# Performance work log

Measured on AMD Instinct MI355X. Metric: run time of the kernel, lower is better.

Reference implementation:

```python
import jax, jax.numpy as jnp
import numpy as np

B, E, S = 2, 1024, 2048
H = 16
D_QK = D_V = D_OUT = 1024
NEG = -1e4


def setup_inputs() -> dict:
    key = jax.random.key(0)
    ks = jax.random.split(key, 12)
    q = jax.random.normal(ks[0], (B, E, 1, S), jnp.float32)
    k = jax.random.normal(ks[1], (B, E, 1, S), jnp.float32)
    v = jax.random.normal(ks[2], (B, E, 1, S), jnp.float32)
    # causal qk_mask: (B, src, 1, tgt); src index > tgt index is masked
    causal = jnp.where(jnp.arange(S)[:, None] > jnp.arange(S)[None, :], NEG, 0.0).astype(jnp.float32)
    qk_mask = jnp.broadcast_to(causal[None, :, None, :], (B, S, 1, S))
    k_mask = jnp.zeros((B, S, 1, 1), jnp.float32)
    sc = 1.0 / np.sqrt(E)
    Wq = jax.random.normal(ks[3], (D_QK, E), jnp.float32) * sc
    Wk = jax.random.normal(ks[4], (D_QK, E), jnp.float32) * sc
    Wv = jax.random.normal(ks[5], (D_V, E), jnp.float32) * sc
    Wo = jax.random.normal(ks[6], (D_OUT, D_V), jnp.float32) * sc
    bq = jnp.zeros((D_QK,), jnp.float32)
    bk = jnp.zeros((D_QK,), jnp.float32)
    bv = jnp.zeros((D_V,), jnp.float32)
    bo = jnp.zeros((D_OUT,), jnp.float32)
    return {"q": q, "k": k, "v": v, "qk_mask": qk_mask, "k_mask": k_mask,
            "Wq": Wq, "bq": bq, "Wk": Wk, "bk": bk, "Wv": Wv, "bv": bv,
            "Wo": Wo, "bo": bo}


def reference(q, k, v, qk_mask, k_mask, Wq, bq, Wk, bk, Wv, bv, Wo, bo):
    b, _, _, tq = q.shape
    sk = k.shape[3]
    d_qk, d_v = Wq.shape[0], Wv.shape[0]
    dh, dvh = d_qk // H, d_v // H
    fact = float(dh) ** (-0.5)
    # 1x1 conv projections on (B, C, 1, S) == matmul over channels
    qp = jnp.einsum('oc,bcis->bois', Wq, q) + bq[None, :, None, None]
    kp = jnp.einsum('oc,bcis->bois', Wk, k) + bk[None, :, None, None]
    vp = jnp.einsum('oc,bcis->bois', Wv, v) + bv[None, :, None, None]
    # split heads: channel dim is head-major (contiguous chunks)
    qh = qp[:, :, 0, :].reshape(b, H, dh, tq)
    kh = kp[:, :, 0, :].reshape(b, H, dh, sk)
    vh = vp[:, :, 0, :].reshape(b, H, dvh, sk)
    # scores: (B, H, src, tgt); masks broadcast over heads
    scores = jnp.einsum('bhcq,bhck->bhkq', qh, kh) * fact
    scores = scores + qk_mask[:, None, :, 0, :] + k_mask[:, None, :, 0, 0][..., None]
    w = jax.nn.softmax(scores, axis=2)  # softmax over src (k) axis
    attn = jnp.einsum('bhkq,bhck->bhcq', w, vh).reshape(b, d_v, 1, tq)
    out = jnp.einsum('oc,bcis->bois', Wo, attn) + bo[None, :, None, None]
    return out
```

## Files before the change

### kernel.cpp

```cpp
#include <hip/hip_runtime.h>
#include <hip/hip_bf16.h>
#include <stdint.h>

typedef unsigned short u16;
typedef __attribute__((ext_vector_type(8))) short short8;
typedef __attribute__((ext_vector_type(4))) short short4v;
typedef __attribute__((ext_vector_type(4))) float f32x4;

#define MFMA16(a,b,c) __builtin_amdgcn_mfma_f32_16x16x32_bf16((a),(b),(c),0,0,0)
#define EXP2F(x) __builtin_amdgcn_exp2f(x)

typedef const __attribute__((address_space(1))) void glb_void;
typedef __attribute__((address_space(3))) void lds_void;

__device__ __forceinline__ u16 f2b(float f){
  unsigned u = __float_as_uint(f);
  u += 0x7fffu + ((u>>16)&1u);
  return (u16)(u>>16);
}
__device__ __forceinline__ unsigned pack_bf16(float a, float b){
  __hip_bfloat162 h = __float22bfloat162_rn(make_float2(a,b));
  unsigned u; __builtin_memcpy(&u, &h, 4); return u;
}
__device__ __forceinline__ void gld16(const void* g, void* l){
  __builtin_amdgcn_global_load_lds((glb_void*)g, (lds_void*)l, 16, 0, 0);
}

__device__ __forceinline__ void stage128x64_sw(const u16* g, u16* lds, int gstride, int w, int lane){
  const int sub = lane>>3, c16 = lane&7;
  const int gcol = (c16 ^ sub)<<3;
  #pragma unroll
  for (int i=0;i<4;++i){
    int r0 = (w*4+i)*8;
    gld16(g + (size_t)(r0 + sub)*gstride + gcol, lds + r0*64);
  }
}
__device__ __forceinline__ void stage64x64_sw(const u16* g, u16* lds, int gstride, int w, int lane){
  const int sub = lane>>3, c16 = lane&7;
  const int gcol = (c16 ^ sub)<<3;
  #pragma unroll
  for (int i=0;i<2;++i){
    int r0 = (w*2+i)*8;
    gld16(g + (size_t)(r0 + sub)*gstride + gcol, lds + r0*64);
  }
}
__device__ __forceinline__ const short8* frag64(const u16* lds, int row, int c16){
  return (const short8*)(lds + row*64 + ((c16 ^ (row&7))<<3));
}
__device__ __forceinline__ const short8* frag128(const u16* lds, int row, int c16){
  return (const short8*)(lds + row*128 + ((c16 ^ (row&15))<<3));
}

__global__ __launch_bounds__(256) void prep(
    const float* __restrict__ q, const float* __restrict__ k, const float* __restrict__ v,
    const float* __restrict__ qkm, const float* __restrict__ km,
    const float* __restrict__ Wq, const float* __restrict__ Wk,
    const float* __restrict__ Wv, const float* __restrict__ Wo,
    u16* __restrict__ W16, char* __restrict__ classes,
    u16* __restrict__ qT, u16* __restrict__ kT, u16* __restrict__ vT)
{
  __shared__ __align__(16) float t[64][72];
  const int bx = blockIdx.x, tid = threadIdx.x;
  const int S = 2048, E = 1024, nW = E*E;

  if (bx < 2048){
    const int sel = bx>>9, blk = bx&511;
    const float* src = sel==0?Wq : sel==1?Wk : sel==2?Wv : Wo;
    const float sc = (sel==0) ? 0.18033688f : 1.0f;
    u16* dst = W16 + (size_t)sel*nW;
    int i = (blk*256 + tid)*8;
    float4 a = *(const float4*)(src+i);
    float4 b = *(const float4*)(src+i+4);
    short8 o;
    o[0]=(short)f2b(a.x*sc); o[1]=(short)f2b(a.y*sc); o[2]=(short)f2b(a.z*sc); o[3]=(short)f2b(a.w*sc);
    o[4]=(short)f2b(b.x*sc); o[5]=(short)f2b(b.y*sc); o[6]=(short)f2b(b.z*sc); o[7]=(short)f2b(b.w*sc);
    *(short8*)(dst+i) = o;
  } else if (bx < 4096){
    const int tt = bx - 2048;
    const int b = tt>>10, qi = (tt>>5)&31, ki = tt&31;
    const int k0 = ki*64, q0 = qi*64;
    int az = 1, an = 1;
    #pragma unroll
    for (int p=0;p<4;++p){
      int e = tid + p*256;
      int row = e>>4, c4 = (e&15)*4;
      float kmv = km[(size_t)b*S + k0 + row];
      float4 mv = *(const float4*)&qkm[((size_t)b*S + k0 + row)*S + q0 + c4];
      mv.x += kmv; mv.y += kmv; mv.z += kmv; mv.w += kmv;
      az &= (mv.x==0.f) & (mv.y==0.f) & (mv.z==0.f) & (mv.w==0.f);
      an &= (mv.x<-1e3f) & (mv.y<-1e3f) & (mv.z<-1e3f) & (mv.w<-1e3f);
    }
    const int az_all = __syncthreads_and(az);
    const int an_all = __syncthreads_and(an);
    if (tid==0)
      classes[((size_t)b*32 + qi)*32 + ki] = an_all ? 2 : (az_all ? 0 : 1);
  } else {
    const int tt = bx - 4096;
    const int tensor = tt>>10, r = tt&1023;
    const int b = r>>9, rr = r&511;
    const int c0 = (rr>>5)*64, s0 = (rr&31)*64;
    const float* x = tensor==0 ? q : tensor==1 ? k : v;
    u16* xt = tensor==0 ? qT : tensor==1 ? kT : vT;
    #pragma unroll
    for (int p=0;p<4;++p){
      int e = tid + p*256;
      int row = e>>4, c4 = (e&15)*4;
      *(float4*)&t[row][c4] = *(const float4*)&x[((size_t)b*E + c0 + row)*S + s0 + c4];
    }
    __syncthreads();
    #pragma unroll
    for (int p=0;p<2;++p){
      int e = tid + p*256;
      int row = e>>3, col8 = (e&7)*8;
      short8 o;
      #pragma unroll
      for (int u=0;u<8;++u) o[u] = (short)f2b(t[col8+u][row]);
      *(short8*)&xt[((size_t)b*S + s0 + row)*E + c0 + col8] = o;
    }
  }
}

template<bool F32OUT>
__device__ __forceinline__ void gemm_core(
    const u16* __restrict__ A, const u16* __restrict__ Bt, const float* __restrict__ bias,
    float bscale, void* __restrict__ Cv, size_t cbase, int N, int K, int bias_on_m,
    int m0, int n0, u16* As, u16* Bs)
{
  const int tid = threadIdx.x, w = tid>>6, lane = tid&63;
  const int ln = lane&15, quad = lane>>4;
  const int m0w = (w>>1)*64, n0w = (w&1)*64;
  f32x4 acc[4][4];
  #pragma unroll
  for(int i=0;i<4;++i)
    #pragma unroll
    for(int j=0;j<4;++j) acc[i][j] = f32x4{0.f,0.f,0.f,0.f};

  for (int kc=0; kc<K; kc+=64){
    __syncthreads();
    stage128x64_sw(A  + (size_t)m0*K + kc, As, K, w, lane);
    stage128x64_sw(Bt + (size_t)n0*K + kc, Bs, K, w, lane);
    __syncthreads();
    #pragma unroll
    for (int kk=0; kk<64; kk+=32){
      const int c16 = (kk>>3) + quad;
      short8 af[4], bf[4];
      #pragma unroll
      for (int mt=0;mt<4;++mt) af[mt] = *frag64(As, m0w+mt*16+ln, c16);
      #pragma unroll
      for (int nt=0;nt<4;++nt) bf[nt] = *frag64(Bs, n0w+nt*16+ln, c16);
      #pragma unroll
      for (int mt=0;mt<4;++mt)
        #pragma unroll
        for (int nt=0;nt<4;++nt)
          acc[mt][nt] = MFMA16(af[mt], bf[nt], acc[mt][nt]);
    }
  }
  #pragma unroll
  for (int mt=0;mt<4;++mt){
    #pragma unroll
    for (int nt=0;nt<4;++nt){
      const int col = n0 + n0w + nt*16 + ln;
      const float bn = bias_on_m ? 0.f : bias[col]*bscale;
      #pragma unroll
      for (int r=0;r<4;++r){
        const int row = m0 + m0w + mt*16 + quad*4 + r;
        const float bb = bias_on_m ? bias[row]*bscale : bn;
        const float val = acc[mt][nt][r] + bb;
        const size_t idx = cbase + (size_t)row*N + col;
        if (F32OUT) ((float*)Cv)[idx] = val;
        else        ((u16*)Cv)[idx]   = f2b(val);
      }
    }
  }
}

__global__ __launch_bounds__(256,3) void proj(
    const u16* __restrict__ qT, const u16* __restrict__ kT, const u16* __restrict__ vT,
    const u16* __restrict__ W16,
    const float* __restrict__ bq, const float* __restrict__ bk, const float* __restrict__ bv,
    u16* __restrict__ Qb, u16* __restrict__ Kb, u16* __restrict__ Vb)
{
  __shared__ __align__(16) u16 As[128*64];
  __shared__ __align__(16) u16 Bs[128*64];
  const int bx = blockIdx.x;
  const int zone = bx>>7, r = bx&127;
  const size_t sSE = (size_t)2048*1024;
  const int nW = 1024*1024;
  if (zone < 4){
    const int sel = zone>>1, b = zone&1;
    const int m0 = (r>>3)*128, n0 = (r&7)*128;
    gemm_core<false>((sel? kT : qT) + b*sSE, W16 + (size_t)sel*nW, sel? bk : bq,
                     sel? 1.0f : 0.18033688f, sel? Kb : Qb, b*sSE,
                     1024, 1024, 0, m0, n0, As, Bs);
  } else {
    const int b = zone&1;
    const int m0 = (r>>4)*128, n0 = (r&15)*128;
    gemm_core<false>(W16 + (size_t)2*nW, vT + b*sSE, bv,
                     1.0f, Vb, b*sSE,
                     2048, 1024, 1, m0, n0, As, Bs);
  }
}

__global__ __launch_bounds__(256,4) void gemm_out64(
    const u16* __restrict__ Wo16, const u16* __restrict__ At, const float* __restrict__ bo,
    float* __restrict__ out)
{
  __shared__ __align__(16) u16 As[64*64];
  __shared__ __align__(16) u16 Bs[128*64];
  const int b = blockIdx.z;
  const int m0 = blockIdx.y*64, n0 = blockIdx.x*128;
  const size_t sSE = (size_t)2048*1024;
  const int K = 1024, N = 2048;
  const u16* Bt = At + b*sSE;
  const int tid = threadIdx.x, w = tid>>6, lane = tid&63;
  const int ln = lane&15, quad = lane>>4;
  const int m0w = (w>>1)*32, n0w = (w&1)*64;
  f32x4 acc[2][4];
  #pragma unroll
  for(int i=0;i<2;++i)
    #pragma unroll
    for(int j=0;j<4;++j) acc[i][j] = f32x4{0.f,0.f,0.f,0.f};

  for (int kc=0; kc<K; kc+=64){
    __syncthreads();
    stage64x64_sw (Wo16 + (size_t)m0*K + kc, As, K, w, lane);
    stage128x64_sw(Bt   + (size_t)n0*K + kc, Bs, K, w, lane);
    __syncthreads();
    #pragma unroll
    for (int kk=0; kk<64; kk+=32){
      const int c16 = (kk>>3) + quad;
      short8 af[2], bf[4];
      #pragma unroll
      for (int mt=0;mt<2;++mt) af[mt] = *frag64(As, m0w+mt*16+ln, c16);
      #pragma unroll
      for (int nt=0;nt<4;++nt) bf[nt] = *frag64(Bs, n0w+nt*16+ln, c16);
      #pragma unroll
      for (int mt=0;mt<2;++mt)
        #pragma unroll
        for (int nt=0;nt<4;++nt)
          acc[mt][nt] = MFMA16(af[mt], bf[nt], acc[mt][nt]);
    }
  }
  #pragma unroll
  for (int mt=0;mt<2;++mt){
    #pragma unroll
    for (int nt=0;nt<4;++nt){
      const int col = n0 + n0w + nt*16 + ln;
      #pragma unroll
      for (int r=0;r<4;++r){
        const int row = m0 + m0w + mt*16 + quad*4 + r;
        out[b*sSE + (size_t)row*N + col] = acc[mt][nt][r] + bo[row];
      }
    }
  }
}

__global__ __launch_bounds__(256,2) void attn(
    const u16* __restrict__ Qb, const u16* __restrict__ Kb, const u16* __restrict__ Vb,
    const float* __restrict__ qk_mask, const float* __restrict__ k_mask,
    const char* __restrict__ classes, u16* __restrict__ Ot)
{
  __shared__ __align__(16) u16 Ks[128*64];
  __shared__ __align__(16) u16 Vs[64*128];
  const int x = blockIdx.x;
  const int b = x&1, h = (x>>1)&15;
  const int pp = x>>5, pair = pp>>1, half = pp&1;
  const int tid = threadIdx.x, w = tid>>6, lane = tid&63;
  const int ln = lane&15, quad = lane>>4;
  const int S = 2048;
  const float LOG2E = 1.44269504f, C2 = 16.0f;

  const int qtA = 15-pair, qtB = pair;
  const int qgA = qtA*128 + half*64 + w*16 + ln;
  const int qgB = qtB*128 + half*64 + w*16 + ln;
  short8 qfA[2], qfB[2];
  #pragma unroll
  for (int kkI=0;kkI<2;++kkI){
    qfA[kkI] = *(const short8*)&Qb[((size_t)b*S + qgA)*1024 + h*64 + kkI*32 + quad*8];
    qfB[kkI] = *(const short8*)&Qb[((size_t)b*S + qgB)*1024 + h*64 + kkI*32 + quad*8];
  }
  const char* clA = classes + ((size_t)b*32 + qtA*2 + half)*32;
  const char* clB = classes + ((size_t)b*32 + qtB*2 + half)*32;

  unsigned mA=0, mB=0;
  #pragma unroll
  for (int kt=0;kt<16;++kt){
    if (!((clA[2*kt]==2) & (clA[2*kt+1]==2))) mA |= 1u<<kt;
    if (!((clB[2*kt]==2) & (clB[2*kt+1]==2))) mB |= 1u<<kt;
  }
  const unsigned mS = mA|mB;

  float rsA=0.f, rsB=0.f;
  f32x4 accA[4], accB[4];
  #pragma unroll
  for (int ct=0;ct<4;++ct){ accA[ct]=f32x4{0.f,0.f,0.f,0.f}; accB[ct]=f32x4{0.f,0.f,0.f,0.f}; }

  const u16* gK = Kb + ((size_t)b*S)*1024 + h*64;
  const u16* gV = Vb + ((size_t)b*1024 + h*64)*S;
  const int subK = lane>>3, cK = ((lane&7)^subK)<<3;
  const int subV = lane>>4, cV0 = lane&15;

  short8 kreg[4], vreg[4];
  auto issue = [&](int kt){
    const int k0 = kt*128;
    #pragma unroll
    for (int i=0;i<4;++i){
      const int r = (w*4+i)*8 + subK;
      kreg[i] = *(const short8*)(gK + (size_t)(k0 + r)*1024 + cK);
    }
    #pragma unroll
    for (int i=0;i<4;++i){
      const int row = (w*4+i)*4 + subV;
      vreg[i] = *(const short8*)(gV + (size_t)row*S + k0 + ((cV0 ^ (row&15))<<3));
    }
  };
  auto write_lds = [&](){
    #pragma unroll
    for (int i=0;i<4;++i)
      *(short8*)&Ks[(w*4+i)*512 + lane*8] = kreg[i];
    #pragma unroll
    for (int i=0;i<4;++i)
      *(short8*)&Vs[(w*4+i)*512 + lane*8] = vreg[i];
  };

  auto compute = [&](const short8* qf, const char* cl, int kt, int qg, float& rs, f32x4* acc){
    const char c0 = cl[2*kt], c1 = cl[2*kt+1];
    const bool nomask = (c0|c1)==0;
    const int k0 = kt*128;
    unsigned pk[8][2];
    #pragma unroll
    for (int t=0;t<8;++t){
      f32x4 s = f32x4{0.f,0.f,0.f,0.f};
      #pragma unroll
      for (int kkI=0;kkI<2;++kkI)
        s = MFMA16(*frag64(Ks, t*16+ln, kkI*4 + quad), qf[kkI], s);
      float e[4];
      if (nomask){
        #pragma unroll
        for (int r=0;r<4;++r) e[r] = EXP2F(s[r] - C2);
      } else {
        #pragma unroll
        for (int r=0;r<4;++r){
          const int kg = k0 + t*16 + quad*4 + r;
          const float m = qk_mask[((size_t)b*S + kg)*S + qg] + k_mask[(size_t)b*S + kg];
          e[r] = EXP2F(fmaf(m, LOG2E, s[r]) - C2);
        }
      }
      rs += (e[0]+e[1]) + (e[2]+e[3]);
      pk[t][0] = pack_bf16(e[0], e[1]);
      pk[t][1] = pack_bf16(e[2], e[3]);
    }
    const int srcA = (quad&1)*32 + ln, srcB = srcA + 16;
    const bool hi = (quad>>1)&1;
    #pragma unroll
    for (int c=0;c<4;++c){
      unsigned a0 = __shfl((int)pk[2*c][0],   srcA, 64);
      unsigned a1 = __shfl((int)pk[2*c][1],   srcA, 64);
      unsigned a2 = __shfl((int)pk[2*c][0],   srcB, 64);
      unsigned a3 = __shfl((int)pk[2*c][1],   srcB, 64);
      unsigned b0 = __shfl((int)pk[2*c+1][0], srcA, 64);
      unsigned b1 = __shfl((int)pk[2*c+1][1], srcA, 64);
      unsigned b2 = __shfl((int)pk[2*c+1][0], srcB, 64);
      unsigned b3 = __shfl((int)pk[2*c+1][1], srcB, 64);
      short8 pf;
      ((unsigned*)&pf)[0] = hi ? b0 : a0;
      ((unsigned*)&pf)[1] = hi ? b1 : a1;
      ((unsigned*)&pf)[2] = hi ? b2 : a2;
      ((unsigned*)&pf)[3] = hi ? b3 : a3;
      __builtin_amdgcn_s_setprio(1);
      #pragma unroll
      for (int ct=0;ct<4;++ct)
        acc[ct] = MFMA16(*frag128(Vs, ct*16+ln, c*4 + quad), pf, acc[ct]);
      __builtin_amdgcn_s_setprio(0);
    }
  };

  int cur = mS ? (__ffs(mS)-1) : 16;
  if (cur < 16) issue(cur);
  while (cur < 16){
    const unsigned above = mS & (0xfffffffeu << cur);
    const int nxt = above ? (__ffs(above)-1) : 16;
    __builtin_amdgcn_s_barrier();
    __builtin_amdgcn_sched_barrier(0);
    write_lds();
    if (nxt < 16) issue(nxt);
    asm volatile("s_waitcnt lgkmcnt(0)" ::: "memory");
    __builtin_amdgcn_s_barrier();
    __builtin_amdgcn_sched_barrier(0);
    if ((mA>>cur)&1) compute(qfA, clA, cur, qgA, rsA, accA);
    if ((mB>>cur)&1) compute(qfB, clB, cur, qgB, rsB, accB);
    cur = nxt;
  }

  auto epi = [&](float rs, f32x4* acc, int qg){
    rs += __shfl_xor(rs, 16, 64);
    rs += __shfl_xor(rs, 32, 64);
    const float rinv = 1.0f / rs;
    #pragma unroll
    for (int ct=0;ct<4;++ct){
      short4v o4;
      #pragma unroll
      for (int r=0;r<4;++r) o4[r] = (short)f2b(acc[ct][r] * rinv);
      *(short4v*)&Ot[((size_t)b*S + qg)*1024 + h*64 + ct*16 + quad*4] = o4;
    }
  };
  epi(rsA, accA, qgA);
  epi(rsB, accB, qgB);
}

extern "C" void kernel_launch(void* const* d_in, const int* in_sizes, int n_in,
                              void* d_out, int out_size, void* d_ws, size_t ws_size,
                              hipStream_t stream)
{
  const float* q   = (const float*)d_in[0];
  const float* k   = (const float*)d_in[1];
  const float* v   = (const float*)d_in[2];
  const float* qkm = (const float*)d_in[3];
  const float* km  = (const float*)d_in[4];
  const float* Wq  = (const float*)d_in[5];
  const float* bq  = (const float*)d_in[6];
  const float* Wk  = (const float*)d_in[7];
  const float* bk  = (const float*)d_in[8];
  const float* Wv  = (const float*)d_in[9];
  const float* bv  = (const float*)d_in[10];
  const float* Wo  = (const float*)d_in[11];
  const float* bo  = (const float*)d_in[12];
  float* out = (float*)d_out;

  const size_t nAct = (size_t)2*2048*1024;
  const int   nW   = 1024*1024;

  u16* A0 = (u16*)d_ws;
  u16* A1 = A0 + nAct;
  u16* A2 = A1 + nAct;
  u16* A3 = A2 + nAct;
  u16* A4 = A3 + nAct;
  u16* A5 = A4 + nAct;
  u16* W16 = A5 + nAct;
  char* classes = (char*)(W16 + (size_t)4*nW);
  u16* Wo16 = W16 + (size_t)3*nW;

  dim3 blk(256);
  prep      <<<dim3(7168), blk, 0, stream>>>(q, k, v, qkm, km, Wq, Wk, Wv, Wo,
                                             W16, classes, A0, A1, A2);
  proj      <<<dim3(768),  blk, 0, stream>>>(A0, A1, A2, W16, bq, bk, bv, A3, A4, A5);
  attn      <<<dim3(512),  blk, 0, stream>>>(A3, A4, A5, qkm, km, classes, A0);
  gemm_out64<<<dim3(16,16,2), blk, 0, stream>>>(Wo16, A0, bo, out);
}
```

Baseline: 242.9 us.

## Split attention q-tile pair across two wave groups in 512-thread blocks

The attention block grows from 256 to 512 threads. The first four waves handle the heavy query tile (A) and the second four handle the light tile (B), instead of every wave computing both tiles serially. K/V staging into LDS is shared across all eight waves, so each wave loads half as much and holds a single accumulator set, which lowers register pressure. The risk is imbalance: the B-group waves sit idle at barriers while the A-group processes its longer causal range, and 512-thread blocks with launch bounds of 4 may constrain occupancy differently.

```diff
diff --git a/kernel.cpp b/kernel.cpp
--- a/kernel.cpp
+++ b/kernel.cpp
@@ -255,7 +255,7 @@
   }
 }
 
-__global__ __launch_bounds__(256,2) void attn(
+__global__ __launch_bounds__(512,4) void attn(
     const u16* __restrict__ Qb, const u16* __restrict__ Kb, const u16* __restrict__ Vb,
     const float* __restrict__ qk_mask, const float* __restrict__ k_mask,
     const char* __restrict__ classes, u16* __restrict__ Ot)
@@ -266,21 +266,22 @@
   const int b = x&1, h = (x>>1)&15;
   const int pp = x>>5, pair = pp>>1, half = pp&1;
   const int tid = threadIdx.x, w = tid>>6, lane = tid&63;
+  const int group = w>>2, wq = w&3;
   const int ln = lane&15, quad = lane>>4;
   const int S = 2048;
   const float LOG2E = 1.44269504f, C2 = 16.0f;
 
   const int qtA = 15-pair, qtB = pair;
-  const int qgA = qtA*128 + half*64 + w*16 + ln;
-  const int qgB = qtB*128 + half*64 + w*16 + ln;
-  short8 qfA[2], qfB[2];
-  #pragma unroll
-  for (int kkI=0;kkI<2;++kkI){
-    qfA[kkI] = *(const short8*)&Qb[((size_t)b*S + qgA)*1024 + h*64 + kkI*32 + quad*8];
-    qfB[kkI] = *(const short8*)&Qb[((size_t)b*S + qgB)*1024 + h*64 + kkI*32 + quad*8];
-  }
+  const int qt = group ? qtB : qtA;
+  const int qg = qt*128 + half*64 + wq*16 + ln;
+  short8 qf[2];
+  #pragma unroll
+  for (int kkI=0;kkI<2;++kkI)
+    qf[kkI] = *(const short8*)&Qb[((size_t)b*S + qg)*1024 + h*64 + kkI*32 + quad*8];
+
   const char* clA = classes + ((size_t)b*32 + qtA*2 + half)*32;
   const char* clB = classes + ((size_t)b*32 + qtB*2 + half)*32;
+  const char* cl  = group ? clB : clA;
 
   unsigned mA=0, mB=0;
   #pragma unroll
@@ -289,41 +290,42 @@
     if (!((clB[2*kt]==2) & (clB[2*kt+1]==2))) mB |= 1u<<kt;
   }
   const unsigned mS = mA|mB;
-
-  float rsA=0.f, rsB=0.f;
-  f32x4 accA[4], accB[4];
-  #pragma unroll
-  for (int ct=0;ct<4;++ct){ accA[ct]=f32x4{0.f,0.f,0.f,0.f}; accB[ct]=f32x4{0.f,0.f,0.f,0.f}; }
+  const unsigned mMe = group ? mB : mA;
+
+  float rs = 0.f;
+  f32x4 acc[4];
+  #pragma unroll
+  for (int ct=0;ct<4;++ct) acc[ct] = f32x4{0.f,0.f,0.f,0.f};
 
   const u16* gK = Kb + ((size_t)b*S)*1024 + h*64;
   const u16* gV = Vb + ((size_t)b*1024 + h*64)*S;
   const int subK = lane>>3, cK = ((lane&7)^subK)<<3;
   const int subV = lane>>4, cV0 = lane&15;
 
-  short8 kreg[4], vreg[4];
+  short8 kreg[2], vreg[2];
   auto issue = [&](int kt){
     const int k0 = kt*128;
     #pragma unroll
-    for (int i=0;i<4;++i){
-      const int r = (w*4+i)*8 + subK;
+    for (int i=0;i<2;++i){
+      const int r = (w*2+i)*8 + subK;
       kreg[i] = *(const short8*)(gK + (size_t)(k0 + r)*1024 + cK);
     }
     #pragma unroll
-    for (int i=0;i<4;++i){
-      const int row = (w*4+i)*4 + subV;
+    for (int i=0;i<2;++i){
+      const int row = (w*2+i)*4 + subV;
       vreg[i] = *(const short8*)(gV + (size_t)row*S + k0 + ((cV0 ^ (row&15))<<3));
     }
   };
   auto write_lds = [&](){
     #pragma unroll
-    for (int i=0;i<4;++i)
-      *(short8*)&Ks[(w*4+i)*512 + lane*8] = kreg[i];
-    #pragma unroll
-    for (int i=0;i<4;++i)
-      *(short8*)&Vs[(w*4+i)*512 + lane*8] = vreg[i];
+    for (int i=0;i<2;++i)
+      *(short8*)&Ks[(w*2+i)*512 + lane*8] = kreg[i];
+    #pragma unroll
+    for (int i=0;i<2;++i)
+      *(short8*)&Vs[(w*2+i)*512 + lane*8] = vreg[i];
   };
 
-  auto compute = [&](const short8* qf, const char* cl, int kt, int qg, float& rs, f32x4* acc){
+  auto compute = [&](int kt){
     const char c0 = cl[2*kt], c1 = cl[2*kt+1];
     const bool nomask = (c0|c1)==0;
     const int k0 = kt*128;
@@ -387,25 +389,20 @@
     asm volatile("s_waitcnt lgkmcnt(0)" ::: "memory");
     __builtin_amdgcn_s_barrier();
     __builtin_amdgcn_sched_barrier(0);
-    if ((mA>>cur)&1) compute(qfA, clA, cur, qgA, rsA, accA);
-    if ((mB>>cur)&1) compute(qfB, clB, cur, qgB, rsB, accB);
+    if ((mMe>>cur)&1) compute(cur);
     cur = nxt;
   }
 
-  auto epi = [&](float rs, f32x4* acc, int qg){
-    rs += __shfl_xor(rs, 16, 64);
-    rs += __shfl_xor(rs, 32, 64);
-    const float rinv = 1.0f / rs;
-    #pragma unroll
-    for (int ct=0;ct<4;++ct){
-      short4v o4;
-      #pragma unroll
-      for (int r=0;r<4;++r) o4[r] = (short)f2b(acc[ct][r] * rinv);
-      *(short4v*)&Ot[((size_t)b*S + qg)*1024 + h*64 + ct*16 + quad*4] = o4;
-    }
-  };
-  epi(rsA, accA, qgA);
-  epi(rsB, accB, qgB);
+  rs += __shfl_xor(rs, 16, 64);
+  rs += __shfl_xor(rs, 32, 64);
+  const float rinv = 1.0f / rs;
+  #pragma unroll
+  for (int ct=0;ct<4;++ct){
+    short4v o4;
+    #pragma unroll
+    for (int r=0;r<4;++r) o4[r] = (short)f2b(acc[ct][r] * rinv);
+    *(short4v*)&Ot[((size_t)b*S + qg)*1024 + h*64 + ct*16 + quad*4] = o4;
+  }
 }
 
 extern "C" void kernel_launch(void* const* d_in, const int* in_sizes, int n_in,
@@ -444,6 +441,6 @@
   prep      <<<dim3(7168), blk, 0, stream>>>(q, k, v, qkm, km, Wq, Wk, Wv, Wo,
                                              W16, classes, A0, A1, A2);
   proj      <<<dim3(768),  blk, 0, stream>>>(A0, A1, A2, W16, bq, bk, bv, A3, A4, A5);
-  attn      <<<dim3(512),  blk, 0, stream>>>(A3, A4, A5, qkm, km, classes, A0);
+  attn      <<<dim3(512),  dim3(512), 0, stream>>>(A3, A4, A5, qkm, km, classes, A0);
   gemm_out64<<<dim3(16,16,2), blk, 0, stream>>>(Wo16, A0, bo, out);
 }
```

Measured after the change: 258.7 us. +6.5%, slower.

## Assign contiguous 128-query tile per block and share K/V fragments across two query groups

Applied to the files above, without the earlier changes.

Previously each block handled two query tiles paired for causal load balance (tile 15-p and tile p), computing each with separate LDS fragment reads. Now each block owns one 128-query tile, and each wave processes two adjacent 16-query groups that share the same K and V fragment loads, interleaving their MFMAs. Grid ordering schedules the heaviest tiles first. This cuts LDS reads per MFMA and skips more masked key tiles, but gives up the paired load balancing and raises register pressure from doubled score and accumulator state.

```diff
diff --git a/kernel.cpp b/kernel.cpp
--- a/kernel.cpp
+++ b/kernel.cpp
@@ -262,33 +262,33 @@
 {
   __shared__ __align__(16) u16 Ks[128*64];
   __shared__ __align__(16) u16 Vs[64*128];
-  const int x = blockIdx.x;
-  const int b = x&1, h = (x>>1)&15;
-  const int pp = x>>5, pair = pp>>1, half = pp&1;
+  const int bx = blockIdx.x;
+  const int pair = 15 - (bx>>5);
+  const int bh = bx & 31;
+  const int b = bh & 1, h = bh >> 1;
   const int tid = threadIdx.x, w = tid>>6, lane = tid&63;
   const int ln = lane&15, quad = lane>>4;
   const int S = 2048;
   const float LOG2E = 1.44269504f, C2 = 16.0f;
 
-  const int qtA = 15-pair, qtB = pair;
-  const int qgA = qtA*128 + half*64 + w*16 + ln;
-  const int qgB = qtB*128 + half*64 + w*16 + ln;
+  const int qgA = pair*128 + w*32 + ln;
+  const int qgB = qgA + 16;
   short8 qfA[2], qfB[2];
   #pragma unroll
   for (int kkI=0;kkI<2;++kkI){
     qfA[kkI] = *(const short8*)&Qb[((size_t)b*S + qgA)*1024 + h*64 + kkI*32 + quad*8];
     qfB[kkI] = *(const short8*)&Qb[((size_t)b*S + qgB)*1024 + h*64 + kkI*32 + quad*8];
   }
-  const char* clA = classes + ((size_t)b*32 + qtA*2 + half)*32;
-  const char* clB = classes + ((size_t)b*32 + qtB*2 + half)*32;
-
-  unsigned mA=0, mB=0;
+
+  const int stw = pair*2 + (w>>1);
+  const char* cl  = classes + ((size_t)b*32 + stw)*32;
+  const char* clH = classes + ((size_t)b*32 + pair*2 + 1)*32;
+  unsigned mW=0, mU=0;
   #pragma unroll
   for (int kt=0;kt<16;++kt){
-    if (!((clA[2*kt]==2) & (clA[2*kt+1]==2))) mA |= 1u<<kt;
-    if (!((clB[2*kt]==2) & (clB[2*kt+1]==2))) mB |= 1u<<kt;
-  }
-  const unsigned mS = mA|mB;
+    if (!((cl [2*kt]==2) & (cl [2*kt+1]==2))) mW |= 1u<<kt;
+    if (!((clH[2*kt]==2) & (clH[2*kt+1]==2))) mU |= 1u<<kt;
+  }
 
   float rsA=0.f, rsB=0.f;
   f32x4 accA[4], accB[4];
@@ -323,62 +323,91 @@
       *(short8*)&Vs[(w*4+i)*512 + lane*8] = vreg[i];
   };
 
-  auto compute = [&](const short8* qf, const char* cl, int kt, int qg, float& rs, f32x4* acc){
+  auto compute = [&](int kt){
     const char c0 = cl[2*kt], c1 = cl[2*kt+1];
     const bool nomask = (c0|c1)==0;
     const int k0 = kt*128;
-    unsigned pk[8][2];
+    unsigned pkA[8][2], pkB[8][2];
     #pragma unroll
     for (int t=0;t<8;++t){
-      f32x4 s = f32x4{0.f,0.f,0.f,0.f};
-      #pragma unroll
-      for (int kkI=0;kkI<2;++kkI)
-        s = MFMA16(*frag64(Ks, t*16+ln, kkI*4 + quad), qf[kkI], s);
-      float e[4];
+      f32x4 sA = f32x4{0.f,0.f,0.f,0.f};
+      f32x4 sB = f32x4{0.f,0.f,0.f,0.f};
+      #pragma unroll
+      for (int kkI=0;kkI<2;++kkI){
+        const short8 af = *frag64(Ks, t*16+ln, kkI*4 + quad);
+        sA = MFMA16(af, qfA[kkI], sA);
+        sB = MFMA16(af, qfB[kkI], sB);
+      }
+      float eA[4], eB[4];
       if (nomask){
         #pragma unroll
-        for (int r=0;r<4;++r) e[r] = EXP2F(s[r] - C2);
+        for (int r=0;r<4;++r){ eA[r] = EXP2F(sA[r] - C2); eB[r] = EXP2F(sB[r] - C2); }
       } else {
         #pragma unroll
         for (int r=0;r<4;++r){
           const int kg = k0 + t*16 + quad*4 + r;
-          const float m = qk_mask[((size_t)b*S + kg)*S + qg] + k_mask[(size_t)b*S + kg];
-          e[r] = EXP2F(fmaf(m, LOG2E, s[r]) - C2);
+          const float kmv = k_mask[(size_t)b*S + kg];
+          const float mA = qk_mask[((size_t)b*S + kg)*S + qgA] + kmv;
+          const float mB = qk_mask[((size_t)b*S + kg)*S + qgB] + kmv;
+          eA[r] = EXP2F(fmaf(mA, LOG2E, sA[r]) - C2);
+          eB[r] = EXP2F(fmaf(mB, LOG2E, sB[r]) - C2);
         }
       }
-      rs += (e[0]+e[1]) + (e[2]+e[3]);
-      pk[t][0] = pack_bf16(e[0], e[1]);
-      pk[t][1] = pack_bf16(e[2], e[3]);
+      rsA += (eA[0]+eA[1]) + (eA[2]+eA[3]);
+      rsB += (eB[0]+eB[1]) + (eB[2]+eB[3]);
+      pkA[t][0] = pack_bf16(eA[0], eA[1]);
+      pkA[t][1] = pack_bf16(eA[2], eA[3]);
+      pkB[t][0] = pack_bf16(eB[0], eB[1]);
+      pkB[t][1] = pack_bf16(eB[2], eB[3]);
     }
     const int srcA = (quad&1)*32 + ln, srcB = srcA + 16;
     const bool hi = (quad>>1)&1;
     #pragma unroll
     for (int c=0;c<4;++c){
-      unsigned a0 = __shfl((int)pk[2*c][0],   srcA, 64);
-      unsigned a1 = __shfl((int)pk[2*c][1],   srcA, 64);
-      unsigned a2 = __shfl((int)pk[2*c][0],   srcB, 64);
-      unsigned a3 = __shfl((int)pk[2*c][1],   srcB, 64);
-      unsigned b0 = __shfl((int)pk[2*c+1][0], srcA, 64);
-      unsigned b1 = __shfl((int)pk[2*c+1][1], srcA, 64);
-      unsigned b2 = __shfl((int)pk[2*c+1][0], srcB, 64);
-      unsigned b3 = __shfl((int)pk[2*c+1][1], srcB, 64);
-      short8 pf;
-      ((unsigned*)&pf)[0] = hi ? b0 : a0;
-      ((unsigned*)&pf)[1] = hi ? b1 : a1;
-      ((unsigned*)&pf)[2] = hi ? b2 : a2;
-      ((unsigned*)&pf)[3] = hi ? b3 : a3;
+      short8 pfA, pfB;
+      {
+        unsigned a0 = __shfl((int)pkA[2*c][0],   srcA, 64);
+        unsigned a1 = __shfl((int)pkA[2*c][1],   srcA, 64);
+        unsigned a2 = __shfl((int)pkA[2*c][0],   srcB, 64);
+        unsigned a3 = __shfl((int)pkA[2*c][1],   srcB, 64);
+        unsigned b0 = __shfl((int)pkA[2*c+1][0], srcA, 64);
+        unsigned b1 = __shfl((int)pkA[2*c+1][1], srcA, 64);
+        unsigned b2 = __shfl((int)pkA[2*c+1][0], srcB, 64);
+        unsigned b3 = __shfl((int)pkA[2*c+1][1], srcB, 64);
+        ((unsigned*)&pfA)[0] = hi ? b0 : a0;
+        ((unsigned*)&pfA)[1] = hi ? b1 : a1;
+        ((unsigned*)&pfA)[2] = hi ? b2 : a2;
+        ((unsigned*)&pfA)[3] = hi ? b3 : a3;
+      }
+      {
+        unsigned a0 = __shfl((int)pkB[2*c][0],   srcA, 64);
+        unsigned a1 = __shfl((int)pkB[2*c][1],   srcA, 64);
+        unsigned a2 = __shfl((int)pkB[2*c][0],   srcB, 64);
+        unsigned a3 = __shfl((int)pkB[2*c][1],   srcB, 64);
+        unsigned b0 = __shfl((int)pkB[2*c+1][0], srcA, 64);
+        unsigned b1 = __shfl((int)pkB[2*c+1][1], srcA, 64);
+        unsigned b2 = __shfl((int)pkB[2*c+1][0], srcB, 64);
+        unsigned b3 = __shfl((int)pkB[2*c+1][1], srcB, 64);
+        ((unsigned*)&pfB)[0] = hi ? b0 : a0;
+        ((unsigned*)&pfB)[1] = hi ? b1 : a1;
+        ((unsigned*)&pfB)[2] = hi ? b2 : a2;
+        ((unsigned*)&pfB)[3] = hi ? b3 : a3;
+      }
       __builtin_amdgcn_s_setprio(1);
       #pragma unroll
-      for (int ct=0;ct<4;++ct)
-        acc[ct] = MFMA16(*frag128(Vs, ct*16+ln, c*4 + quad), pf, acc[ct]);
+      for (int ct=0;ct<4;++ct){
+        const short8 vf = *frag128(Vs, ct*16+ln, c*4 + quad);
+        accA[ct] = MFMA16(vf, pfA, accA[ct]);
+        accB[ct] = MFMA16(vf, pfB, accB[ct]);
+      }
       __builtin_amdgcn_s_setprio(0);
     }
   };
 
-  int cur = mS ? (__ffs(mS)-1) : 16;
+  int cur = mU ? (__ffs(mU)-1) : 16;
   if (cur < 16) issue(cur);
   while (cur < 16){
-    const unsigned above = mS & (0xfffffffeu << cur);
+    const unsigned above = mU & (0xfffffffeu << cur);
     const int nxt = above ? (__ffs(above)-1) : 16;
     __builtin_amdgcn_s_barrier();
     __builtin_amdgcn_sched_barrier(0);
@@ -387,25 +416,26 @@
     asm volatile("s_waitcnt lgkmcnt(0)" ::: "memory");
     __builtin_amdgcn_s_barrier();
     __builtin_amdgcn_sched_barrier(0);
-    if ((mA>>cur)&1) compute(qfA, clA, cur, qgA, rsA, accA);
-    if ((mB>>cur)&1) compute(qfB, clB, cur, qgB, rsB, accB);
+    if ((mW>>cur)&1) compute(cur);
     cur = nxt;
   }
 
-  auto epi = [&](float rs, f32x4* acc, int qg){
-    rs += __shfl_xor(rs, 16, 64);
-    rs += __shfl_xor(rs, 32, 64);
-    const float rinv = 1.0f / rs;
-    #pragma unroll
-    for (int ct=0;ct<4;++ct){
-      short4v o4;
-      #pragma unroll
-      for (int r=0;r<4;++r) o4[r] = (short)f2b(acc[ct][r] * rinv);
-      *(short4v*)&Ot[((size_t)b*S + qg)*1024 + h*64 + ct*16 + quad*4] = o4;
-    }
-  };
-  epi(rsA, accA, qgA);
-  epi(rsB, accB, qgB);
+  rsA += __shfl_xor(rsA, 16, 64);
+  rsA += __shfl_xor(rsA, 32, 64);
+  rsB += __shfl_xor(rsB, 16, 64);
+  rsB += __shfl_xor(rsB, 32, 64);
+  const float rinvA = 1.0f / rsA, rinvB = 1.0f / rsB;
+  #pragma unroll
+  for (int ct=0;ct<4;++ct){
+    short4v oA, oB;
+    #pragma unroll
+    for (int r=0;r<4;++r){
+      oA[r] = (short)f2b(accA[ct][r] * rinvA);
+      oB[r] = (short)f2b(accB[ct][r] * rinvB);
+    }
+    *(short4v*)&Ot[((size_t)b*S + qgA)*1024 + h*64 + ct*16 + quad*4] = oA;
+    *(short4v*)&Ot[((size_t)b*S + qgB)*1024 + h*64 + ct*16 + quad*4] = oB;
+  }
 }
 
 extern "C" void kernel_launch(void* const* d_in, const int* in_sizes, int n_in,
```

After: 259.6 us. 1.07x slower.
